# Performance work log

Measured on AMD Instinct MI355X. Metric: run time of the kernel, lower is better.

## Reference

```python
import jax, jax.numpy as jnp
import numpy as np

D_MODEL = 512
NEG = -1e9


def setup_inputs() -> dict:
    key = jax.random.key(0)
    ks = jax.random.split(key, 8)
    B, S, D = 8, 2048, D_MODEL
    scale = 1.0 / np.sqrt(D)
    x = jax.random.normal(ks[0], (B, S, D), dtype=jnp.float32)
    event_lengths = jax.random.randint(ks[1], (B,), 1, S + 1)
    Wq = jax.random.normal(ks[2], (D, D), dtype=jnp.float32) * scale
    bq = jax.random.normal(ks[3], (D,), dtype=jnp.float32) * 0.01
    Wk = jax.random.normal(ks[4], (D, D), dtype=jnp.float32) * scale
    bk = jax.random.normal(ks[5], (D,), dtype=jnp.float32) * 0.01
    Wv = jax.random.normal(ks[6], (D, D), dtype=jnp.float32) * scale
    bv = jax.random.normal(ks[7], (D,), dtype=jnp.float32) * 0.01
    return {"x": x, "event_lengths": event_lengths, "Wq": Wq, "bq": bq,
            "Wk": Wk, "bk": bk, "Wv": Wv, "bv": bv}


def reference(x, event_lengths, Wq, bq, Wk, bk, Wv, bv):
    B, S, D = x.shape
    inv_scale = 1.0 / jnp.sqrt(jnp.float32(D))
    # torch nn.Linear: y = x @ W^T + b
    q = jnp.einsum('bsd,ed->bse', x, Wq) + bq
    k = jnp.einsum('bsd,ed->bse', x, Wk) + bk
    v = jnp.einsum('bsd,ed->bse', x, Wv) + bv
    scores = jnp.einsum('bqd,bkd->bqk', q, k) * inv_scale  # [B,S,S]
    idx = jnp.arange(S)
    L = event_lengths[:, None, None]  # [B,1,1]
    mask = (idx[None, :, None] < L) & (idx[None, None, :] < L)  # [B,S,S]
    scores = jnp.where(mask, scores, NEG)
    attn = jax.nn.softmax(scores, axis=-1)
    # dropout is identity at eval time
    return jnp.einsum('bqk,bkd->bqd', attn, v)
```

## Files before the change

kernel.cpp:

```cpp
#include <hip/hip_runtime.h>
#include <hip/hip_bf16.h>
#include <cstdint>

#define DEV static __device__ __forceinline__

typedef __attribute__((ext_vector_type(8))) short bf16x8;
typedef __attribute__((ext_vector_type(4))) float f32x4;
typedef __attribute__((ext_vector_type(4))) float float4v;
typedef __attribute__((ext_vector_type(8))) unsigned short us8;
typedef __attribute__((ext_vector_type(4))) unsigned short us4;

constexpr int SEQ = 2048;
constexpr int DM = 512;
constexpr float INV_SCALE = 0.044194173824159216f;
constexpr float LOG2E = 1.4426950408889634f;
constexpr float SEXP = INV_SCALE * LOG2E;

DEV unsigned short f2bf(float f) {
  unsigned int u = __float_as_uint(f);
  u = u + 0x7FFFu + ((u >> 16) & 1u);
  return (unsigned short)(u >> 16);
}
DEV float bf2f(unsigned short h) { return __uint_as_float(((unsigned int)h) << 16); }

DEV void gload_lds16(const void* g, void* l) {
  __builtin_amdgcn_global_load_lds(
      (const __attribute__((address_space(1))) void*)g,
      (__attribute__((address_space(3))) void*)l, 16, 0, 0);
}

__global__ void convert_x_kernel(const float* __restrict__ x, unsigned short* __restrict__ xb) {
  int64_t i = ((int64_t)blockIdx.x * 256 + threadIdx.x) * 8;
  float4v a = *(const float4v*)(x + i);
  float4v b = *(const float4v*)(x + i + 4);
  us8 o;
  o[0] = f2bf(a[0]); o[1] = f2bf(a[1]); o[2] = f2bf(a[2]); o[3] = f2bf(a[3]);
  o[4] = f2bf(b[0]); o[5] = f2bf(b[1]); o[6] = f2bf(b[2]); o[7] = f2bf(b[3]);
  *(us8*)(xb + i) = o;
}

__global__ void convert_w_kernel(const float* __restrict__ wq, const float* __restrict__ wk,
                                 const float* __restrict__ wv, unsigned short* __restrict__ wb) {
  int w = blockIdx.x >> 8;
  int blk = blockIdx.x & 255;
  const float* src = (w == 0) ? wq : ((w == 1) ? wk : wv);
  int i = (blk * 256 + (int)threadIdx.x) * 4;
  float4v a = *(const float4v*)(src + i);
  us4 o;
  o[0] = f2bf(a[0]); o[1] = f2bf(a[1]); o[2] = f2bf(a[2]); o[3] = f2bf(a[3]);
  *(us4*)(wb + (w << 18) + i) = o;
}

__global__ __launch_bounds__(256) void qkv_gemm_kernel(
    const unsigned short* __restrict__ xb, const unsigned short* __restrict__ wb,
    const float* __restrict__ bq, const float* __restrict__ bk, const float* __restrict__ bv,
    unsigned short* __restrict__ Qb, unsigned short* __restrict__ Kb,
    unsigned short* __restrict__ VTb)
{
  const int bid = blockIdx.x;
  const int eidx = bid >> 3;
  const int mrow = ((bid & 7) << 4) | (eidx & 15);
  const int wn = eidx >> 4;
  const int which = wn >> 2;
  const int m0 = mrow << 7;
  const int n0 = (wn & 3) << 7;
  const unsigned short* W = wb + ((int64_t)which << 18);
  const int tid = threadIdx.x;
  const int lane = tid & 63, wid = tid >> 6;
  const int lo = lane & 15, hi = lane >> 4;
  const int wrow = wid >> 1, wcol = wid & 1;

  __shared__ alignas(16) unsigned short lA[128 * 64];
  __shared__ alignas(16) unsigned short lB[128 * 64];

  f32x4 acc[4][4];
  #pragma unroll
  for (int i = 0; i < 4; ++i)
    #pragma unroll
    for (int j = 0; j < 4; ++j) acc[i][j] = (f32x4){0.f, 0.f, 0.f, 0.f};

  for (int k0 = 0; k0 < 512; k0 += 64) {
    if (k0) __syncthreads();
    #pragma unroll
    for (int i = 0; i < 4; ++i) {
      const int m = (i << 8) + tid;
      const int mw = (i << 8) + (wid << 6);
      const int row = m >> 3, c = m & 7;
      const int ca = c ^ (row & 7);
      gload_lds16(xb + ((int64_t)(m0 + row) << 9) + k0 + (ca << 3), lA + (mw << 3));
      gload_lds16(W  + ((int64_t)(n0 + row) << 9) + k0 + (ca << 3), lB + (mw << 3));
    }
    __syncthreads();

    #pragma unroll
    for (int ks = 0; ks < 2; ++ks) {
      bf16x8 af[4], bfr[4];
      #pragma unroll
      for (int mf = 0; mf < 4; ++mf) {
        const int row = (wrow << 6) + (mf << 4) + lo;
        const int cc = ((ks << 2) + hi) ^ (row & 7);
        af[mf] = *(const bf16x8*)(lA + (row << 6) + (cc << 3));
      }
      #pragma unroll
      for (int nf = 0; nf < 4; ++nf) {
        const int row = (wcol << 6) + (nf << 4) + lo;
        const int cc = ((ks << 2) + hi) ^ (row & 7);
        bfr[nf] = *(const bf16x8*)(lB + (row << 6) + (cc << 3));
      }
      #pragma unroll
      for (int mf = 0; mf < 4; ++mf)
        #pragma unroll
        for (int nf = 0; nf < 4; ++nf)
          acc[mf][nf] = __builtin_amdgcn_mfma_f32_16x16x32_bf16(af[mf], bfr[nf], acc[mf][nf], 0, 0, 0);
    }
  }

  const float* bias = (which == 0) ? bq : ((which == 1) ? bk : bv);
  if (which < 2) {
    unsigned short* outp = (which == 0) ? Qb : Kb;
    #pragma unroll
    for (int nf = 0; nf < 4; ++nf) {
      const int e = n0 + (wcol << 6) + (nf << 4) + lo;
      const float bb = bias[e];
      #pragma unroll
      for (int mf = 0; mf < 4; ++mf) {
        const int rowg = m0 + (wrow << 6) + (mf << 4) + (hi << 2);
        #pragma unroll
        for (int r = 0; r < 4; ++r)
          outp[((int64_t)(rowg + r) << 9) + e] = f2bf(acc[mf][nf][r] + bb);
      }
    }
  } else {
    #pragma unroll
    for (int nf = 0; nf < 4; ++nf) {
      const int e = n0 + (wcol << 6) + (nf << 4) + lo;
      const float bb = bias[e];
      #pragma unroll
      for (int mf = 0; mf < 4; ++mf) {
        const int rowg = m0 + (wrow << 6) + (mf << 4) + (hi << 2);
        const int bidx = rowg >> 11;
        const int s = rowg & 2047;
        us4 pk;
        pk[0] = f2bf(acc[mf][nf][0] + bb);
        pk[1] = f2bf(acc[mf][nf][1] + bb);
        pk[2] = f2bf(acc[mf][nf][2] + bb);
        pk[3] = f2bf(acc[mf][nf][3] + bb);
        *(us4*)(VTb + (((int64_t)(bidx << 9) + e) << 11) + s) = pk;
      }
    }
  }
}

__global__ void vmean_kernel(const unsigned short* __restrict__ VTb, float* __restrict__ vmean) {
  const int row = blockIdx.x;
  const unsigned short* src = VTb + (int64_t)row * SEQ;
  const int tid = threadIdx.x;
  us8 v = *(const us8*)(src + tid * 8);
  float s = 0.f;
  #pragma unroll
  for (int j = 0; j < 8; ++j) s += bf2f(v[j]);
  #pragma unroll
  for (int off = 1; off < 64; off <<= 1) s += __shfl_xor(s, off);
  __shared__ float ps[4];
  const int lane = tid & 63, wid = tid >> 6;
  if (lane == 0) ps[wid] = s;
  __syncthreads();
  if (tid == 0) vmean[row] = (ps[0] + ps[1] + ps[2] + ps[3]) * (1.f / 2048.f);
}

__global__ __launch_bounds__(256) void score_gemm_kernel(
    const unsigned short* __restrict__ Qb, const unsigned short* __restrict__ Kb,
    const int* __restrict__ ev, unsigned short* __restrict__ P, int b0)
{
  const int z = blockIdx.z;
  const int b = b0 + z;
  const int L = ev[b];
  const int q0 = blockIdx.x << 7;
  const int k0g = blockIdx.y << 7;
  if (q0 >= L || k0g >= L) return;

  const unsigned short* Qrows = Qb + ((int64_t)b << 20);
  const unsigned short* Krows = Kb + ((int64_t)b << 20);
  const int tid = threadIdx.x;
  const int lane = tid & 63, wid = tid >> 6;
  const int lo = lane & 15, hi = lane >> 4;
  const int wrow = wid >> 1, wcol = wid & 1;

  __shared__ alignas(16) unsigned short lA[128 * 64];
  __shared__ alignas(16) unsigned short lB[128 * 64];

  f32x4 acc[4][4];
  #pragma unroll
  for (int i = 0; i < 4; ++i)
    #pragma unroll
    for (int j = 0; j < 4; ++j) acc[i][j] = (f32x4){0.f, 0.f, 0.f, 0.f};

  for (int k0 = 0; k0 < 512; k0 += 64) {
    if (k0) __syncthreads();
    #pragma unroll
    for (int i = 0; i < 4; ++i) {
      const int m = (i << 8) + tid;
      const int mw = (i << 8) + (wid << 6);
      const int row = m >> 3, c = m & 7;
      const int ca = c ^ (row & 7);
      gload_lds16(Qrows + ((int64_t)(q0 + row) << 9) + k0 + (ca << 3), lA + (mw << 3));
      gload_lds16(Krows + ((int64_t)(k0g + row) << 9) + k0 + (ca << 3), lB + (mw << 3));
    }
    __syncthreads();

    #pragma unroll
    for (int ks = 0; ks < 2; ++ks) {
      bf16x8 af[4], bfr[4];
      #pragma unroll
      for (int mf = 0; mf < 4; ++mf) {
        const int row = (wrow << 6) + (mf << 4) + lo;
        const int cc = ((ks << 2) + hi) ^ (row & 7);
        af[mf] = *(const bf16x8*)(lA + (row << 6) + (cc << 3));
      }
      #pragma unroll
      for (int nf = 0; nf < 4; ++nf) {
        const int row = (wcol << 6) + (nf << 4) + lo;
        const int cc = ((ks << 2) + hi) ^ (row & 7);
        bfr[nf] = *(const bf16x8*)(lB + (row << 6) + (cc << 3));
      }
      #pragma unroll
      for (int mf = 0; mf < 4; ++mf)
        #pragma unroll
        for (int nf = 0; nf < 4; ++nf)
          acc[mf][nf] = __builtin_amdgcn_mfma_f32_16x16x32_bf16(af[mf], bfr[nf], acc[mf][nf], 0, 0, 0);
    }
  }

  unsigned short* Pz = P + ((int64_t)z << 22);
  #pragma unroll
  for (int nf = 0; nf < 4; ++nf) {
    const int kcol = k0g + (wcol << 6) + (nf << 4) + lo;
    const bool kok = kcol < L;
    #pragma unroll
    for (int mf = 0; mf < 4; ++mf) {
      const int rowg = q0 + (wrow << 6) + (mf << 4) + (hi << 2);
      #pragma unroll
      for (int r = 0; r < 4; ++r) {
        const float p = (kok && (rowg + r < L)) ? exp2f(acc[mf][nf][r] * SEXP) : 0.f;
        Pz[((int64_t)(rowg + r) << 11) + kcol] = f2bf(p);
      }
    }
  }
}

__global__ __launch_bounds__(256) void pv_gemm_kernel(
    const unsigned short* __restrict__ P, const unsigned short* __restrict__ VTb,
    const float* __restrict__ vmean, const int* __restrict__ ev,
    float* __restrict__ out, int b0)
{
  const int z = blockIdx.z;
  const int b = b0 + z;
  const int L = ev[b];
  const int q0 = blockIdx.x << 6;
  const int d0 = blockIdx.y << 7;
  const int tid = threadIdx.x;

  float* outb = out + ((int64_t)b << 20);
  const float* vm = vmean + (b << 9);

  if (q0 >= L) {
    #pragma unroll
    for (int j = 0; j < 8; ++j) {
      const int idx = tid + (j << 8);
      const int r = idx >> 5, c = (idx & 31) << 2;
      *(float4v*)(outb + ((int64_t)(q0 + r) << 9) + d0 + c) = *(const float4v*)(vm + d0 + c);
    }
    return;
  }

  const int lane = tid & 63, wid = tid >> 6;
  const int lo = lane & 15, hi = lane >> 4;
  const int wrow = wid >> 1, wcol = wid & 1;

  __shared__ alignas(16) unsigned short lA[2][64 * 64];
  __shared__ alignas(16) unsigned short lB[2][128 * 64];
  __shared__ float lpart[64][4];

  const unsigned short* Pz = P + ((int64_t)z << 22);
  const unsigned short* Vrows = VTb + ((int64_t)(b << 9) << 11);

  f32x4 acc[2][4];
  #pragma unroll
  for (int i = 0; i < 2; ++i)
    #pragma unroll
    for (int j = 0; j < 4; ++j) acc[i][j] = (f32x4){0.f, 0.f, 0.f, 0.f};
  float ls[2] = {0.f, 0.f};

  const int nk = (L + 63) >> 6;

  auto stage = [&](int cur, int kk) {
    #pragma unroll
    for (int i = 0; i < 2; ++i) {
      const int m = (i << 8) + tid;
      const int mw = (i << 8) + (wid << 6);
      const int row = m >> 3, c = m & 7;
      const int ca = c ^ (row & 7);
      gload_lds16(Pz + ((int64_t)(q0 + row) << 11) + (kk << 6) + (ca << 3),
                  &lA[cur][mw << 3]);
    }
    #pragma unroll
    for (int i = 0; i < 4; ++i) {
      const int m = (i << 8) + tid;
      const int mw = (i << 8) + (wid << 6);
      const int row = m >> 3, c = m & 7;
      const int ca = c ^ (row & 7);
      gload_lds16(Vrows + ((int64_t)(d0 + row) << 11) + (kk << 6) + (ca << 3),
                  &lB[cur][mw << 3]);
    }
  };

  stage(0, 0);
  __syncthreads();
  int cur = 0;

  for (int kk = 0; kk < nk; ++kk) {
    if (kk + 1 < nk) stage(cur ^ 1, kk + 1);

    #pragma unroll
    for (int ks = 0; ks < 2; ++ks) {
      bf16x8 af[2], bfr[4];
      #pragma unroll
      for (int mf = 0; mf < 2; ++mf) {
        const int row = (wrow << 5) + (mf << 4) + lo;
        const int cc = ((ks << 2) + hi) ^ (row & 7);
        af[mf] = *(const bf16x8*)(&lA[cur][(row << 6) + (cc << 3)]);
      }
      #pragma unroll
      for (int nf = 0; nf < 4; ++nf) {
        const int row = (wcol << 6) + (nf << 4) + lo;
        const int cc = ((ks << 2) + hi) ^ (row & 7);
        bfr[nf] = *(const bf16x8*)(&lB[cur][(row << 6) + (cc << 3)]);
      }
      if (wcol == 0) {
        #pragma unroll
        for (int mf = 0; mf < 2; ++mf) {
          float t = 0.f;
          #pragma unroll
          for (int j = 0; j < 8; ++j) t += bf2f((unsigned short)af[mf][j]);
          ls[mf] += t;
        }
      }
      #pragma unroll
      for (int mf = 0; mf < 2; ++mf)
        #pragma unroll
        for (int nf = 0; nf < 4; ++nf)
          acc[mf][nf] = __builtin_amdgcn_mfma_f32_16x16x32_bf16(af[mf], bfr[nf], acc[mf][nf], 0, 0, 0);
    }

    __syncthreads();
    cur ^= 1;
  }

  if (wcol == 0) {
    #pragma unroll
    for (int mf = 0; mf < 2; ++mf)
      lpart[(wrow << 5) + (mf << 4) + lo][hi] = ls[mf];
  }
  __syncthreads();

  #pragma unroll
  for (int mf = 0; mf < 2; ++mf) {
    const int rowb = (wrow << 5) + (mf << 4) + (hi << 2);
    float rl[4];
    #pragma unroll
    for (int r = 0; r < 4; ++r) {
      const float l = lpart[rowb + r][0] + lpart[rowb + r][1] +
                      lpart[rowb + r][2] + lpart[rowb + r][3];
      rl[r] = 1.0f / l;
    }
    #pragma unroll
    for (int nf = 0; nf < 4; ++nf) {
      const int col = d0 + (wcol << 6) + (nf << 4) + lo;
      const float vmc = vm[col];
      #pragma unroll
      for (int r = 0; r < 4; ++r) {
        const int rowg = q0 + rowb + r;
        const float val = (rowg < L) ? (acc[mf][nf][r] * rl[r]) : vmc;
        outb[((int64_t)rowg << 9) + col] = val;
      }
    }
  }
}

extern "C" void kernel_launch(void* const* d_in, const int* in_sizes, int n_in,
                              void* d_out, int out_size, void* d_ws, size_t ws_size,
                              hipStream_t stream) {
  const float* x  = (const float*)d_in[0];
  const int* ev   = (const int*)d_in[1];
  const float* Wq = (const float*)d_in[2];
  const float* bq = (const float*)d_in[3];
  const float* Wk = (const float*)d_in[4];
  const float* bk = (const float*)d_in[5];
  const float* Wv = (const float*)d_in[6];
  const float* bv = (const float*)d_in[7];
  float* out = (float*)d_out;

  unsigned short* xb  = (unsigned short*)d_ws;
  unsigned short* wb  = xb + (int64_t)16384 * 512;
  unsigned short* Qb  = wb + 3 * 512 * 512;
  unsigned short* Kb  = Qb + (int64_t)16384 * 512;
  unsigned short* VTb = Kb + (int64_t)16384 * 512;
  float* vmean = (float*)(VTb + (int64_t)16384 * 512);
  unsigned short* Ptail = (unsigned short*)(vmean + 8 * 512);

  const size_t base_bytes = (size_t)((char*)Ptail - (char*)d_ws);
  const size_t pbytes = (size_t)SEQ * SEQ * 2;
  int nb;
  unsigned short* P;
  if (ws_size >= base_bytes + 8 * pbytes)      { nb = 8; P = Ptail; }
  else if (ws_size >= base_bytes + 4 * pbytes) { nb = 4; P = Ptail; }
  else                                         { nb = 2; P = xb; }

  convert_x_kernel<<<4096, 256, 0, stream>>>(x, xb);
  convert_w_kernel<<<768, 256, 0, stream>>>(Wq, Wk, Wv, wb);
  qkv_gemm_kernel<<<1536, 256, 0, stream>>>(xb, wb, bq, bk, bv, Qb, Kb, VTb);
  vmean_kernel<<<4096, 256, 0, stream>>>(VTb, vmean);

  for (int c = 0; c < 8 / nb; ++c) {
    score_gemm_kernel<<<dim3(16, 16, nb), 256, 0, stream>>>(Qb, Kb, ev, P, c * nb);
    pv_gemm_kernel<<<dim3(32, 4, nb), 256, 0, stream>>>(P, VTb, vmean, ev, out, c * nb);
  }
}
```

Before: 120.9 us.

## Widen GEMM tiles to 128x256 and use 128-deep single-buffered PV k-steps

Result: slower. 153.3 us (+26.8%).

```diff
diff --git a/kernel.cpp b/kernel.cpp
--- a/kernel.cpp
+++ b/kernel.cpp
@@ -61,9 +61,9 @@
   const int eidx = bid >> 3;
   const int mrow = ((bid & 7) << 4) | (eidx & 15);
   const int wn = eidx >> 4;
-  const int which = wn >> 2;
+  const int which = wn >> 1;
   const int m0 = mrow << 7;
-  const int n0 = (wn & 3) << 7;
+  const int n0 = (wn & 1) << 8;
   const unsigned short* W = wb + ((int64_t)which << 18);
   const int tid = threadIdx.x;
   const int lane = tid & 63, wid = tid >> 6;
@@ -71,13 +71,13 @@
   const int wrow = wid >> 1, wcol = wid & 1;
 
   __shared__ alignas(16) unsigned short lA[128 * 64];
-  __shared__ alignas(16) unsigned short lB[128 * 64];
-
-  f32x4 acc[4][4];
+  __shared__ alignas(16) unsigned short lB[256 * 64];
+
+  f32x4 acc[4][8];
   #pragma unroll
   for (int i = 0; i < 4; ++i)
     #pragma unroll
-    for (int j = 0; j < 4; ++j) acc[i][j] = (f32x4){0.f, 0.f, 0.f, 0.f};
+    for (int j = 0; j < 8; ++j) acc[i][j] = (f32x4){0.f, 0.f, 0.f, 0.f};
 
   for (int k0 = 0; k0 < 512; k0 += 64) {
     if (k0) __syncthreads();
@@ -88,13 +88,20 @@
       const int row = m >> 3, c = m & 7;
       const int ca = c ^ (row & 7);
       gload_lds16(xb + ((int64_t)(m0 + row) << 9) + k0 + (ca << 3), lA + (mw << 3));
-      gload_lds16(W  + ((int64_t)(n0 + row) << 9) + k0 + (ca << 3), lB + (mw << 3));
+    }
+    #pragma unroll
+    for (int i = 0; i < 8; ++i) {
+      const int m = (i << 8) + tid;
+      const int mw = (i << 8) + (wid << 6);
+      const int row = m >> 3, c = m & 7;
+      const int ca = c ^ (row & 7);
+      gload_lds16(W + ((int64_t)(n0 + row) << 9) + k0 + (ca << 3), lB + (mw << 3));
     }
     __syncthreads();
 
     #pragma unroll
     for (int ks = 0; ks < 2; ++ks) {
-      bf16x8 af[4], bfr[4];
+      bf16x8 af[4], bfr[8];
       #pragma unroll
       for (int mf = 0; mf < 4; ++mf) {
         const int row = (wrow << 6) + (mf << 4) + lo;
@@ -102,15 +109,15 @@
         af[mf] = *(const bf16x8*)(lA + (row << 6) + (cc << 3));
       }
       #pragma unroll
-      for (int nf = 0; nf < 4; ++nf) {
-        const int row = (wcol << 6) + (nf << 4) + lo;
+      for (int nf = 0; nf < 8; ++nf) {
+        const int row = (wcol << 7) + (nf << 4) + lo;
         const int cc = ((ks << 2) + hi) ^ (row & 7);
         bfr[nf] = *(const bf16x8*)(lB + (row << 6) + (cc << 3));
       }
       #pragma unroll
       for (int mf = 0; mf < 4; ++mf)
         #pragma unroll
-        for (int nf = 0; nf < 4; ++nf)
+        for (int nf = 0; nf < 8; ++nf)
           acc[mf][nf] = __builtin_amdgcn_mfma_f32_16x16x32_bf16(af[mf], bfr[nf], acc[mf][nf], 0, 0, 0);
     }
   }
@@ -119,8 +126,8 @@
   if (which < 2) {
     unsigned short* outp = (which == 0) ? Qb : Kb;
     #pragma unroll
-    for (int nf = 0; nf < 4; ++nf) {
-      const int e = n0 + (wcol << 6) + (nf << 4) + lo;
+    for (int nf = 0; nf < 8; ++nf) {
+      const int e = n0 + (wcol << 7) + (nf << 4) + lo;
       const float bb = bias[e];
       #pragma unroll
       for (int mf = 0; mf < 4; ++mf) {
@@ -132,8 +139,8 @@
     }
   } else {
     #pragma unroll
-    for (int nf = 0; nf < 4; ++nf) {
-      const int e = n0 + (wcol << 6) + (nf << 4) + lo;
+    for (int nf = 0; nf < 8; ++nf) {
+      const int e = n0 + (wcol << 7) + (nf << 4) + lo;
       const float bb = bias[e];
       #pragma unroll
       for (int mf = 0; mf < 4; ++mf) {
@@ -176,7 +183,7 @@
   const int b = b0 + z;
   const int L = ev[b];
   const int q0 = blockIdx.x << 7;
-  const int k0g = blockIdx.y << 7;
+  const int k0g = blockIdx.y << 8;
   if (q0 >= L || k0g >= L) return;
 
   const unsigned short* Qrows = Qb + ((int64_t)b << 20);
@@ -187,13 +194,13 @@
   const int wrow = wid >> 1, wcol = wid & 1;
 
   __shared__ alignas(16) unsigned short lA[128 * 64];
-  __shared__ alignas(16) unsigned short lB[128 * 64];
-
-  f32x4 acc[4][4];
+  __shared__ alignas(16) unsigned short lB[256 * 64];
+
+  f32x4 acc[4][8];
   #pragma unroll
   for (int i = 0; i < 4; ++i)
     #pragma unroll
-    for (int j = 0; j < 4; ++j) acc[i][j] = (f32x4){0.f, 0.f, 0.f, 0.f};
+    for (int j = 0; j < 8; ++j) acc[i][j] = (f32x4){0.f, 0.f, 0.f, 0.f};
 
   for (int k0 = 0; k0 < 512; k0 += 64) {
     if (k0) __syncthreads();
@@ -204,13 +211,20 @@
       const int row = m >> 3, c = m & 7;
       const int ca = c ^ (row & 7);
       gload_lds16(Qrows + ((int64_t)(q0 + row) << 9) + k0 + (ca << 3), lA + (mw << 3));
+    }
+    #pragma unroll
+    for (int i = 0; i < 8; ++i) {
+      const int m = (i << 8) + tid;
+      const int mw = (i << 8) + (wid << 6);
+      const int row = m >> 3, c = m & 7;
+      const int ca = c ^ (row & 7);
       gload_lds16(Krows + ((int64_t)(k0g + row) << 9) + k0 + (ca << 3), lB + (mw << 3));
     }
     __syncthreads();
 
     #pragma unroll
     for (int ks = 0; ks < 2; ++ks) {
-      bf16x8 af[4], bfr[4];
+      bf16x8 af[4], bfr[8];
       #pragma unroll
       for (int mf = 0; mf < 4; ++mf) {
         const int row = (wrow << 6) + (mf << 4) + lo;
@@ -218,23 +232,23 @@
         af[mf] = *(const bf16x8*)(lA + (row << 6) + (cc << 3));
       }
       #pragma unroll
-      for (int nf = 0; nf < 4; ++nf) {
-        const int row = (wcol << 6) + (nf << 4) + lo;
+      for (int nf = 0; nf < 8; ++nf) {
+        const int row = (wcol << 7) + (nf << 4) + lo;
         const int cc = ((ks << 2) + hi) ^ (row & 7);
         bfr[nf] = *(const bf16x8*)(lB + (row << 6) + (cc << 3));
       }
       #pragma unroll
       for (int mf = 0; mf < 4; ++mf)
         #pragma unroll
-        for (int nf = 0; nf < 4; ++nf)
+        for (int nf = 0; nf < 8; ++nf)
           acc[mf][nf] = __builtin_amdgcn_mfma_f32_16x16x32_bf16(af[mf], bfr[nf], acc[mf][nf], 0, 0, 0);
     }
   }
 
   unsigned short* Pz = P + ((int64_t)z << 22);
   #pragma unroll
-  for (int nf = 0; nf < 4; ++nf) {
-    const int kcol = k0g + (wcol << 6) + (nf << 4) + lo;
+  for (int nf = 0; nf < 8; ++nf) {
+    const int kcol = k0g + (wcol << 7) + (nf << 4) + lo;
     const bool kok = kcol < L;
     #pragma unroll
     for (int mf = 0; mf < 4; ++mf) {
@@ -277,8 +291,8 @@
   const int lo = lane & 15, hi = lane >> 4;
   const int wrow = wid >> 1, wcol = wid & 1;
 
-  __shared__ alignas(16) unsigned short lA[2][64 * 64];
-  __shared__ alignas(16) unsigned short lB[2][128 * 64];
+  __shared__ alignas(16) unsigned short lA[64 * 128];
+  __shared__ alignas(16) unsigned short lB[128 * 128];
   __shared__ float lpart[64][4];
 
   const unsigned short* Pz = P + ((int64_t)z << 22);
@@ -291,50 +305,43 @@
     for (int j = 0; j < 4; ++j) acc[i][j] = (f32x4){0.f, 0.f, 0.f, 0.f};
   float ls[2] = {0.f, 0.f};
 
-  const int nk = (L + 63) >> 6;
-
-  auto stage = [&](int cur, int kk) {
-    #pragma unroll
-    for (int i = 0; i < 2; ++i) {
-      const int m = (i << 8) + tid;
-      const int mw = (i << 8) + (wid << 6);
-      const int row = m >> 3, c = m & 7;
-      const int ca = c ^ (row & 7);
-      gload_lds16(Pz + ((int64_t)(q0 + row) << 11) + (kk << 6) + (ca << 3),
-                  &lA[cur][mw << 3]);
-    }
+  const int nk = (L + 127) >> 7;
+  for (int kk = 0; kk < nk; ++kk) {
+    if (kk) __syncthreads();
     #pragma unroll
     for (int i = 0; i < 4; ++i) {
       const int m = (i << 8) + tid;
       const int mw = (i << 8) + (wid << 6);
-      const int row = m >> 3, c = m & 7;
-      const int ca = c ^ (row & 7);
-      gload_lds16(Vrows + ((int64_t)(d0 + row) << 11) + (kk << 6) + (ca << 3),
-                  &lB[cur][mw << 3]);
-    }
-  };
-
-  stage(0, 0);
-  __syncthreads();
-  int cur = 0;
-
-  for (int kk = 0; kk < nk; ++kk) {
-    if (kk + 1 < nk) stage(cur ^ 1, kk + 1);
-
-    #pragma unroll
-    for (int ks = 0; ks < 2; ++ks) {
+      const int row = m >> 4, c = m & 15;
+      const int ca = c ^ (row & 15);
+      gload_lds16(Pz + ((int64_t)(q0 + row) << 11) + (kk << 7) + (ca << 3),
+                  lA + (mw << 3));
+    }
+    #pragma unroll
+    for (int i = 0; i < 8; ++i) {
+      const int m = (i << 8) + tid;
+      const int mw = (i << 8) + (wid << 6);
+      const int row = m >> 4, c = m & 15;
+      const int ca = c ^ (row & 15);
+      gload_lds16(Vrows + ((int64_t)(d0 + row) << 11) + (kk << 7) + (ca << 3),
+                  lB + (mw << 3));
+    }
+    __syncthreads();
+
+    #pragma unroll
+    for (int ks = 0; ks < 4; ++ks) {
       bf16x8 af[2], bfr[4];
       #pragma unroll
       for (int mf = 0; mf < 2; ++mf) {
         const int row = (wrow << 5) + (mf << 4) + lo;
-        const int cc = ((ks << 2) + hi) ^ (row & 7);
-        af[mf] = *(const bf16x8*)(&lA[cur][(row << 6) + (cc << 3)]);
+        const int cc = ((ks << 2) + hi) ^ (row & 15);
+        af[mf] = *(const bf16x8*)(lA + (row << 7) + (cc << 3));
       }
       #pragma unroll
       for (int nf = 0; nf < 4; ++nf) {
         const int row = (wcol << 6) + (nf << 4) + lo;
-        const int cc = ((ks << 2) + hi) ^ (row & 7);
-        bfr[nf] = *(const bf16x8*)(&lB[cur][(row << 6) + (cc << 3)]);
+        const int cc = ((ks << 2) + hi) ^ (row & 15);
+        bfr[nf] = *(const bf16x8*)(lB + (row << 7) + (cc << 3));
       }
       if (wcol == 0) {
         #pragma unroll
@@ -351,9 +358,6 @@
         for (int nf = 0; nf < 4; ++nf)
           acc[mf][nf] = __builtin_amdgcn_mfma_f32_16x16x32_bf16(af[mf], bfr[nf], acc[mf][nf], 0, 0, 0);
     }
-
-    __syncthreads();
-    cur ^= 1;
   }
 
   if (wcol == 0) {
@@ -418,11 +422,11 @@
 
   convert_x_kernel<<<4096, 256, 0, stream>>>(x, xb);
   convert_w_kernel<<<768, 256, 0, stream>>>(Wq, Wk, Wv, wb);
-  qkv_gemm_kernel<<<1536, 256, 0, stream>>>(xb, wb, bq, bk, bv, Qb, Kb, VTb);
+  qkv_gemm_kernel<<<768, 256, 0, stream>>>(xb, wb, bq, bk, bv, Qb, Kb, VTb);
   vmean_kernel<<<4096, 256, 0, stream>>>(VTb, vmean);
 
   for (int c = 0; c < 8 / nb; ++c) {
-    score_gemm_kernel<<<dim3(16, 16, nb), 256, 0, stream>>>(Qb, Kb, ev, P, c * nb);
+    score_gemm_kernel<<<dim3(16, 8, nb), 256, 0, stream>>>(Qb, Kb, ev, P, c * nb);
     pv_gemm_kernel<<<dim3(32, 4, nb), 256, 0, stream>>>(P, VTb, vmean, ev, out, c * nb);
   }
 }
```
